# Kernel optimization log

Hardware: AMD Instinct MI355X
Metric: run time of the kernel (lower is better)

The kernel has to match this reference:

```python
import jax, jax.numpy as jnp
import numpy as np

DIM = 2048
H = 16       # num_heads
HKV = 4      # num_kv_heads
HD = DIM // H  # head_dim = 128
REP = H // HKV
ROPE_BASE = 10000.0
QK_GAIN_INIT = 1.0
B, T = 4, 2048


def rms_norm(x):
    # F.rms_norm with eps=None -> machine eps of dtype, no weight
    eps = jnp.finfo(x.dtype).eps
    return x * jax.lax.rsqrt(jnp.mean(x * x, axis=-1, keepdims=True) + eps)


def apply_rotary_emb(x, cos, sin):
    # x: [B, h, T, HD]; cos/sin: [T, HD//2]
    h = x.shape[-1] // 2
    x1, x2 = x[..., :h], x[..., h:]
    return jnp.concatenate((x1 * cos + x2 * sin, -x1 * sin + x2 * cos), axis=-1)


def setup_inputs() -> dict:
    key = jax.random.key(0)
    ks = jax.random.split(key, 6)
    kv_dim = HKV * HD
    x = jax.random.normal(ks[0], (B, T, DIM), dtype=jnp.float32)
    Wq = jax.random.normal(ks[1], (DIM, DIM), dtype=jnp.float32) * 0.02
    Wk = jax.random.normal(ks[2], (kv_dim, DIM), dtype=jnp.float32) * 0.02
    Wv = jax.random.normal(ks[3], (kv_dim, DIM), dtype=jnp.float32) * 0.02
    Wproj = jax.random.normal(ks[4], (DIM, DIM), dtype=jnp.float32) * 0.02
    q_gain = jnp.full((H,), QK_GAIN_INIT, dtype=jnp.float32)
    return {"x": x, "Wq": Wq, "Wk": Wk, "Wv": Wv, "Wproj": Wproj, "q_gain": q_gain}


def reference(x, Wq, Wk, Wv, Wproj, q_gain):
    Bs, Ts, D = x.shape
    # QKV projections (bias-free Linear: x @ W.T)
    q = (x @ Wq.T).reshape(Bs, Ts, H, HD).transpose(0, 2, 1, 3)      # [B,H,T,HD]
    k = (x @ Wk.T).reshape(Bs, Ts, HKV, HD).transpose(0, 2, 1, 3)    # [B,HKV,T,HD]
    v = (x @ Wv.T).reshape(Bs, Ts, HKV, HD).transpose(0, 2, 1, 3)
    # RMSNorm over head_dim
    q, k = rms_norm(q), rms_norm(k)
    # rotary
    inv_freq = 1.0 / (ROPE_BASE ** (jnp.arange(0, HD, 2, dtype=jnp.float32) / HD))
    t = jnp.arange(Ts, dtype=jnp.float32)
    freqs = jnp.outer(t, inv_freq)  # [T, HD//2]
    cos, sin = jnp.cos(freqs), jnp.sin(freqs)
    q = apply_rotary_emb(q, cos, sin)
    k = apply_rotary_emb(k, cos, sin)
    # per-head query gain
    q = q * q_gain[None, :, None, None]
    # GQA attention without materializing repeated K/V
    qg = q.reshape(Bs, HKV, REP, Ts, HD)
    scale = 1.0 / jnp.sqrt(jnp.asarray(HD, dtype=q.dtype))
    scores = jnp.einsum('bgrtd,bgsd->bgrts', qg, k) * scale  # [B,HKV,REP,T,T]
    causal = jnp.tril(jnp.ones((Ts, Ts), dtype=bool))
    scores = jnp.where(causal, scores, jnp.finfo(scores.dtype).min)
    attn = jax.nn.softmax(scores, axis=-1)
    y = jnp.einsum('bgrts,bgsd->bgrtd', attn, v)              # [B,HKV,REP,T,HD]
    y = y.reshape(Bs, H, Ts, HD).transpose(0, 2, 1, 3).reshape(Bs, Ts, D)
    return y @ Wproj.T
```

## Files before the change

kernel.cpp:

```cpp
#include <hip/hip_runtime.h>
#include <stdint.h>

typedef unsigned short u16;
typedef __attribute__((ext_vector_type(4))) float f32x4;
typedef __attribute__((ext_vector_type(8))) __bf16 bf16x8;
typedef __attribute__((ext_vector_type(4))) u16 u16x4;
typedef __attribute__((ext_vector_type(8))) u16 u16x8;

#define T_SEQ 2048
#define NB 4
#define NH 16
#define NKV 4
#define HDIM 128
#define PSTR 72

__device__ __forceinline__ u16 f2bf(float f) {
  __bf16 h = (__bf16)f;
  return __builtin_bit_cast(u16, h);
}
__device__ __forceinline__ float bf2f(u16 u) {
  union { uint32_t u; float f; } v; v.u = ((uint32_t)u) << 16;
  return v.f;
}
__device__ __forceinline__ void gload16(const void* g, void* l) {
  __builtin_amdgcn_global_load_lds((const __attribute__((address_space(1))) void*)g,
                                   (__attribute__((address_space(3))) void*)l, 16, 0, 0);
}
__device__ __forceinline__ f32x4 mfma16(bf16x8 a, bf16x8 b, f32x4 c) {
  return __builtin_amdgcn_mfma_f32_16x16x32_bf16(a, b, c, 0, 0, 0);
}

__global__ __launch_bounds__(256) void cvt_all(const float* __restrict__ x,
                                               const float* __restrict__ wq,
                                               const float* __restrict__ wk,
                                               const float* __restrict__ wv,
                                               const float* __restrict__ wp,
                                               u16* __restrict__ xo, u16* __restrict__ wqo,
                                               u16* __restrict__ wko, u16* __restrict__ wvo,
                                               u16* __restrict__ wpo) {
  const int C_X = 16777216 / 4, C_WQ = 4194304 / 4, C_WKV = 1048576 / 4;
  const int B1 = C_X, B2 = B1 + C_WQ, B3 = B2 + C_WKV, B4 = B3 + C_WKV;
  const int total = B4 + C_WQ;
  int idx = blockIdx.x * 256 + threadIdx.x;
  int stride = gridDim.x * 256;
  for (int c = idx; c < total; c += stride) {
    const float* src;
    u16* dst;
    int off;
    if (c < B1)      { src = x;  dst = xo;  off = c; }
    else if (c < B2) { src = wq; dst = wqo; off = c - B1; }
    else if (c < B3) { src = wk; dst = wko; off = c - B2; }
    else if (c < B4) { src = wv; dst = wvo; off = c - B3; }
    else             { src = wp; dst = wpo; off = c - B4; }
    f32x4 v = *(const f32x4*)(src + (size_t)off * 4);
    u16x4 o;
    o[0] = f2bf(v[0]); o[1] = f2bf(v[1]); o[2] = f2bf(v[2]); o[3] = f2bf(v[3]);
    *(u16x4*)(dst + (size_t)off * 4) = o;
  }
}

template <int MODE>
__global__ __launch_bounds__(256) void gemm128p3(const u16* __restrict__ A,
                                                 const u16* __restrict__ Bt,
                                                 u16* __restrict__ k_o, u16* __restrict__ v_o,
                                                 float* __restrict__ f_o,
                                                 int K, int nx, int cpx) {
  __shared__ __align__(16) u16 As3[3 * 128 * 32];
  __shared__ __align__(16) u16 Bs3[3 * 128 * 32];
  const int tid = threadIdx.x;
  const int l = tid & 63, w = tid >> 6;
  const int l15 = l & 15, g16 = l >> 4;
  const int wr = w >> 1, wc = w & 1;

  const int oid = blockIdx.x + nx * blockIdx.y;
  const int wid = (oid & 7) * cpx + (oid >> 3);
  const int m0 = (wid / nx) * 128, n0 = (wid % nx) * 128;

  f32x4 acc[4][4] = {};

  const int row0 = tid >> 2, row1 = 64 + (tid >> 2), cc = tid & 3;
  const int sc0 = cc ^ ((row0 >> 1) & 3), sc1 = cc ^ ((row1 >> 1) & 3);
  const u16* pA0 = A + (size_t)(m0 + row0) * K + sc0 * 8;
  const u16* pA1 = A + (size_t)(m0 + row1) * K + sc1 * 8;
  const u16* pB0 = Bt + (size_t)(n0 + row0) * K + sc0 * 8;
  const u16* pB1 = Bt + (size_t)(n0 + row1) * K + sc1 * 8;

#define STAGE(buf)                                                   \
  {                                                                  \
    char* ab = (char*)As3 + (buf) * 8192 + w * 1024;                 \
    char* bb = (char*)Bs3 + (buf) * 8192 + w * 1024;                 \
    gload16(pA0, ab);                                                \
    gload16(pA1, ab + 4096);                                         \
    gload16(pB0, bb);                                                \
    gload16(pB1, bb + 4096);                                         \
    pA0 += 32; pA1 += 32; pB0 += 32; pB1 += 32;                      \
  }

#define COMPUTE(buf)                                                 \
  {                                                                  \
    const u16* AsB = As3 + (buf) * 4096;                             \
    const u16* BsB = Bs3 + (buf) * 4096;                             \
    bf16x8 af[4], bfr[4];                                            \
    _Pragma("unroll")                                                \
    for (int mt = 0; mt < 4; ++mt) {                                 \
      int arow = wr * 64 + mt * 16 + l15;                            \
      af[mt] = *(const bf16x8*)&AsB[arow * 32 +                      \
                                    ((g16 ^ ((arow >> 1) & 3)) * 8)];\
    }                                                                \
    _Pragma("unroll")                                                \
    for (int nt = 0; nt < 4; ++nt) {                                 \
      int brow = wc * 64 + nt * 16 + l15;                            \
      bfr[nt] = *(const bf16x8*)&BsB[brow * 32 +                     \
                                     ((g16 ^ ((brow >> 1) & 3)) * 8)];\
    }                                                                \
    __builtin_amdgcn_s_setprio(1);                                   \
    _Pragma("unroll")                                                \
    for (int mt = 0; mt < 4; ++mt)                                   \
      _Pragma("unroll")                                              \
      for (int nt = 0; nt < 4; ++nt)                                 \
        acc[mt][nt] = mfma16(af[mt], bfr[nt], acc[mt][nt]);          \
    __builtin_amdgcn_s_setprio(0);                                   \
  }

  const int ntiles = K >> 5;
  STAGE(0);
  STAGE(1);
  asm volatile("s_waitcnt vmcnt(4)" ::: "memory");
  __builtin_amdgcn_s_barrier();

  int cur = 0, nxt = 2;
  for (int t = 0; t < ntiles; ++t) {
    const bool more2 = (t + 2 < ntiles);
    if (more2) STAGE(nxt);
    COMPUTE(cur);
    if (t + 1 < ntiles) {
      if (more2) {
        asm volatile("s_waitcnt vmcnt(4)" ::: "memory");
      } else {
        asm volatile("s_waitcnt vmcnt(0)" ::: "memory");
      }
      __builtin_amdgcn_s_barrier();
    }
    cur = (cur == 2) ? 0 : cur + 1;
    nxt = (nxt == 2) ? 0 : nxt + 1;
  }
#undef STAGE
#undef COMPUTE

#pragma unroll
  for (int mt = 0; mt < 4; ++mt) {
#pragma unroll
    for (int r = 0; r < 4; ++r) {
      int row = m0 + wr * 64 + mt * 16 + g16 * 4 + r;
#pragma unroll
      for (int nt = 0; nt < 4; ++nt) {
        int n = n0 + wc * 64 + nt * 16 + l15;
        float val = acc[mt][nt][r];
        if (MODE == 1) {
          f_o[(size_t)row * 2048 + n] = val;
        } else {
          int b = row >> 11, t = row & (T_SEQ - 1);
          u16 bv = f2bf(val);
          if (n < 512) {
            int h = n >> 7, d = n & 127;
            k_o[((size_t)(b * NKV + h) * T_SEQ + t) * HDIM + d] = bv;
          } else {
            int n2 = n - 512; int h = n2 >> 7, d = n2 & 127;
            v_o[((size_t)(b * NKV + h) * T_SEQ + t) * HDIM + d] = bv;
          }
        }
      }
    }
  }
}

template <int MODE>
__global__ __launch_bounds__(512, 2) void gemm256(const u16* __restrict__ A,
                                                  const u16* __restrict__ Bt,
                                                  u16* __restrict__ q_o,
                                                  float* __restrict__ f_o,
                                                  int K, int ntn, int cpx) {
  __shared__ __align__(16) u16 As[2][256 * 64];
  __shared__ __align__(16) u16 Bs[2][256 * 64];
  const int tid = threadIdx.x;
  const int l = tid & 63, w = tid >> 6;
  const int l16 = l & 15, g16 = l >> 4;
  const int wr = w >> 2, wc = w & 3;

  const int oid = blockIdx.x;
  const int wid = (oid & 7) * cpx + (oid >> 3);
  const int m0 = (wid / ntn) * 256, n0 = (wid % ntn) * 256;

  f32x4 acc[8][4] = {};

  const int srow = tid >> 3, scc = tid & 7;
  const u16* pA[4];
  const u16* pB[4];
#pragma unroll
  for (int j = 0; j < 4; ++j) {
    int row = j * 64 + srow;
    int cc = scc ^ (row & 7);
    pA[j] = A + (size_t)(m0 + row) * K + cc * 8;
    pB[j] = Bt + (size_t)(n0 + row) * K + cc * 8;
  }

#define STAGE(buf)                                              \
  {                                                             \
    char* ab = (char*)As[buf] + w * 1024;                       \
    char* bb = (char*)Bs[buf] + w * 1024;                       \
    _Pragma("unroll")                                           \
    for (int j = 0; j < 4; ++j) {                               \
      gload16(pA[j], ab + j * 8192);                            \
      pA[j] += 64;                                              \
    }                                                           \
    _Pragma("unroll")                                           \
    for (int j = 0; j < 4; ++j) {                               \
      gload16(pB[j], bb + j * 8192);                            \
      pB[j] += 64;                                              \
    }                                                           \
  }

  const int ntk = K >> 6;
  STAGE(0);
  __syncthreads();

  for (int t = 0; t < ntk; ++t) {
    const int buf = t & 1;
    if (t + 1 < ntk) STAGE(buf ^ 1);
#pragma unroll
    for (int ks = 0; ks < 2; ++ks) {
      bf16x8 bfr[4];
#pragma unroll
      for (int nf = 0; nf < 4; ++nf) {
        int brow = wc * 64 + nf * 16 + l16;
        int slot = (ks * 4 + g16) ^ (brow & 7);
        bfr[nf] = *(const bf16x8*)&Bs[buf][brow * 64 + slot * 8];
      }
#pragma unroll
      for (int rh = 0; rh < 2; ++rh) {
        bf16x8 af[4];
#pragma unroll
        for (int f = 0; f < 4; ++f) {
          int arow = wr * 128 + rh * 64 + f * 16 + l16;
          int slot = (ks * 4 + g16) ^ (arow & 7);
          af[f] = *(const bf16x8*)&As[buf][arow * 64 + slot * 8];
        }
        __builtin_amdgcn_s_setprio(1);
#pragma unroll
        for (int f = 0; f < 4; ++f)
#pragma unroll
          for (int nf = 0; nf < 4; ++nf)
            acc[rh * 4 + f][nf] = mfma16(af[f], bfr[nf], acc[rh * 4 + f][nf]);
        __builtin_amdgcn_s_setprio(0);
      }
    }
    __syncthreads();
  }
#undef STAGE

#pragma unroll
  for (int rf = 0; rf < 8; ++rf) {
#pragma unroll
    for (int rr = 0; rr < 4; ++rr) {
      int row = m0 + wr * 128 + rf * 16 + g16 * 4 + rr;
#pragma unroll
      for (int nf = 0; nf < 4; ++nf) {
        int n = n0 + wc * 64 + nf * 16 + l16;
        float val = acc[rf][nf][rr];
        if (MODE == 1) {
          f_o[(size_t)row * 2048 + n] = val;
        } else {
          int b = row >> 11, t = row & (T_SEQ - 1);
          int h = n >> 7, d = n & 127;
          q_o[((size_t)(b * NH + h) * T_SEQ + t) * HDIM + d] = f2bf(val);
        }
      }
    }
  }
}

__global__ __launch_bounds__(256) void rmsrope(u16* __restrict__ buf,
                                               const float* __restrict__ gains,
                                               int nheads, float fold, int useGain) {
  const int w = threadIdx.x >> 6, l = threadIdx.x & 63;
  const int rid = blockIdx.x * 4 + w;
  const int t = rid & (T_SEQ - 1);
  const int h = (rid >> 11) % nheads;
  u16* p = buf + (size_t)rid * HDIM;
  float x1 = bf2f(p[l]), x2 = bf2f(p[l + 64]);
  float ss = x1 * x1 + x2 * x2;
#pragma unroll
  for (int m = 32; m; m >>= 1) ss += __shfl_xor(ss, m, 64);
  float rn = rsqrtf(ss * (1.0f / 128.0f) + 1.1920928955078125e-7f);
  float g = useGain ? gains[h] * fold : fold;
  float sc = rn * g;
  float inv = exp2f(-(float)l * (13.287712379549449f / 64.0f));
  float ang = (float)t * inv;
  float s, c;
  __sincosf(ang, &s, &c);
  float o1 = (x1 * c + x2 * s) * sc;
  float o2 = (x2 * c - x1 * s) * sc;
  p[l] = f2bf(o1);
  p[l + 64] = f2bf(o2);
}

__global__ __launch_bounds__(256) void vtrans(const u16* __restrict__ in,
                                              u16* __restrict__ out) {
  __shared__ u16 tileT[64][PSTR];
  const int tid = threadIdx.x;
  const int t0 = blockIdx.x * 64, d0 = blockIdx.y * 64, bg = blockIdx.z;
  const int row = tid >> 2, c0 = (tid & 3) * 16;
  const u16* src = in + ((size_t)bg * T_SEQ + t0 + row) * HDIM + d0 + c0;
  u16x8 a = *(const u16x8*)src;
  u16x8 bb = *(const u16x8*)(src + 8);
#pragma unroll
  for (int j = 0; j < 8; ++j) {
    tileT[c0 + j][row] = a[j];
    tileT[c0 + 8 + j][row] = bb[j];
  }
  __syncthreads();
  u16* dst = out + ((size_t)bg * HDIM + d0 + row) * T_SEQ + t0 + c0;
  *(u16x8*)dst = *(const u16x8*)&tileT[row][c0];
  *(u16x8*)(dst + 8) = *(const u16x8*)&tileT[row][c0 + 8];
}

__global__ __launch_bounds__(512) void attn_fwd8(const u16* __restrict__ qb,
                                                 const u16* __restrict__ kb,
                                                 const u16* __restrict__ vtb,
                                                 u16* __restrict__ yb,
                                                 const float* __restrict__ gains) {
  __shared__ __align__(16) u16 Ks[64 * 128];
  __shared__ __align__(16) u16 Vs[128 * 64];
  __shared__ __align__(16) u16 Ps[8][16 * PSTR];

  const int tid = threadIdx.x, l = tid & 63, w = tid >> 6;
  const int l16 = l & 15, g16 = l >> 4;

  const int oid = blockIdx.x + 8 * blockIdx.y;
  const int wid = (oid & 7) * 64 + (oid >> 3);
  const int pair = wid & 7, bh = wid >> 3;
  const int b = bh >> 4, h = bh & 15, gr = h >> 2;

  const float Mh = 16.33f * fabsf(gains[h]) + 0.5f;
  const u16* kbase = kb + (size_t)(b * NKV + gr) * T_SEQ * HDIM;
  const u16* vtbase = vtb + (size_t)(b * NKV + gr) * HDIM * T_SEQ;

  bf16x8 ones;
#pragma unroll
  for (int j = 0; j < 8; ++j) ones[j] = (__bf16)1.0f;

  const int krow0 = tid >> 4, kc0 = tid & 15;
  const int krow1 = 32 + (tid >> 4);
  const u16* kp0_base = kbase + (size_t)krow0 * HDIM + (kc0 ^ (krow0 & 7)) * 8;
  const u16* kp1_base = kbase + (size_t)krow1 * HDIM + (kc0 ^ (krow1 & 7)) * 8;
  const int vrow0 = tid >> 3, vc0 = tid & 7;
  const int vrow1 = 64 + (tid >> 3);
  const u16* vp0_base = vtbase + (size_t)vrow0 * T_SEQ + (vc0 ^ (vrow0 & 7)) * 8;
  const u16* vp1_base = vtbase + (size_t)vrow1 * T_SEQ + (vc0 ^ (vrow1 & 7)) * 8;
  char* kd0 = (char*)Ks + (w * 64) * 16;
  char* kd1 = (char*)Ks + (512 + w * 64) * 16;
  char* vd0 = (char*)Vs + (w * 64) * 16;
  char* vd1 = (char*)Vs + (512 + w * 64) * 16;

  for (int phase = 0; phase < 2; ++phase) {
    const int qt = phase ? (15 - pair) : pair;
    const int q0 = qt * 128 + w * 16;
    const int qhi = q0 + 15;

    bf16x8 qf[4];
    const u16* qbase = qb + ((size_t)bh * T_SEQ + q0) * HDIM;
#pragma unroll
    for (int s = 0; s < 4; ++s)
      qf[s] = *(const bf16x8*)(qbase + (size_t)l16 * HDIM + s * 32 + g16 * 8);

    f32x4 oacc[8] = {};
    f32x4 dden = {};
    const int ntile = 2 * qt + 2;

    const u16* kp0 = kp0_base;
    const u16* kp1 = kp1_base;
    const u16* vp0 = vp0_base;
    const u16* vp1 = vp1_base;

    for (int kt = 0; kt < ntile; ++kt) {
      gload16(kp0, kd0);
      gload16(kp1, kd1);
      gload16(vp0, vd0);
      gload16(vp1, vd1);
      kp0 += 64 * HDIM; kp1 += 64 * HDIM;
      vp0 += 64; vp1 += 64;
      __syncthreads();

      if (kt * 64 <= qhi) {
        f32x4 sacc[4] = {};
        __builtin_amdgcn_s_setprio(1);
#pragma unroll
        for (int mt = 0; mt < 4; ++mt) {
          int key = mt * 16 + l16;
#pragma unroll
          for (int s = 0; s < 4; ++s) {
            bf16x8 kf = *(const bf16x8*)&Ks[key * 128 + ((s * 4 + g16) ^ (key & 7)) * 8];
            sacc[mt] = mfma16(kf, qf[s], sacc[mt]);
          }
        }
        __builtin_amdgcn_s_setprio(0);

        if (kt * 64 + 63 > q0) {
#pragma unroll
          for (int mt = 0; mt < 4; ++mt) {
            int keyb = kt * 64 + mt * 16 + g16 * 4;
            u16x4 p4;
#pragma unroll
            for (int r = 0; r < 4; ++r) {
              float pv = exp2f(sacc[mt][r] - Mh);
              if (keyb + r > q0 + l16) pv = 0.f;
              p4[r] = f2bf(pv);
            }
            *(u16x4*)&Ps[w][l16 * PSTR + mt * 16 + g16 * 4] = p4;
          }
        } else {
#pragma unroll
          for (int mt = 0; mt < 4; ++mt) {
            u16x4 p4;
#pragma unroll
            for (int r = 0; r < 4; ++r)
              p4[r] = f2bf(exp2f(sacc[mt][r] - Mh));
            *(u16x4*)&Ps[w][l16 * PSTR + mt * 16 + g16 * 4] = p4;
          }
        }

        __builtin_amdgcn_s_setprio(1);
#pragma unroll
        for (int ks = 0; ks < 2; ++ks) {
          bf16x8 pa = *(const bf16x8*)&Ps[w][l16 * PSTR + ks * 32 + g16 * 8];
          dden = mfma16(pa, ones, dden);
#pragma unroll
          for (int dt = 0; dt < 8; ++dt) {
            int d = dt * 16 + l16;
            bf16x8 vv = *(const bf16x8*)&Vs[d * 64 + (((ks * 4 + g16) ^ (d & 7)) * 8)];
            oacc[dt] = mfma16(pa, vv, oacc[dt]);
          }
        }
        __builtin_amdgcn_s_setprio(0);
      }
      __syncthreads();
    }

    float rden[4];
#pragma unroll
    for (int r = 0; r < 4; ++r) rden[r] = 1.f / dden[r];

#pragma unroll
    for (int dt = 0; dt < 8; ++dt)
#pragma unroll
      for (int r = 0; r < 4; ++r) {
        int t = q0 + g16 * 4 + r;
        int d = dt * 16 + l16;
        yb[(((size_t)b * T_SEQ + t) * NH + h) * HDIM + d] = f2bf(oacc[dt][r] * rden[r]);
      }
    __syncthreads();
  }
}

extern "C" void kernel_launch(void* const* d_in, const int* in_sizes, int n_in,
                              void* d_out, int out_size, void* d_ws, size_t ws_size,
                              hipStream_t stream) {
  const float* x = (const float*)d_in[0];
  const float* Wq = (const float*)d_in[1];
  const float* Wk = (const float*)d_in[2];
  const float* Wv = (const float*)d_in[3];
  const float* Wproj = (const float*)d_in[4];
  const float* qg = (const float*)d_in[5];
  float* out = (float*)d_out;

  u16* xbf = (u16*)d_ws;
  u16* Wqkv = xbf + (size_t)8192 * 2048;
  u16* Wpj = Wqkv + (size_t)3072 * 2048;
  u16* qbuf = Wpj + (size_t)2048 * 2048;
  u16* kbuf = qbuf + (size_t)8192 * 2048;
  u16* vbuf = kbuf + (size_t)2048 * 2048;
  u16* ybuf = xbf;
  u16* vtbuf = Wqkv;

  cvt_all<<<2048, 256, 0, stream>>>(x, Wq, Wk, Wv, Wproj,
                                    xbf, Wqkv, Wqkv + (size_t)2048 * 2048,
                                    Wqkv + (size_t)2560 * 2048, Wpj);

  gemm256<0><<<256, 512, 0, stream>>>(xbf, Wqkv, qbuf, nullptr, 2048, 8, 32);

  gemm128p3<2><<<dim3(8, 64), 256, 0, stream>>>(xbf, Wqkv + (size_t)2048 * 2048,
                                                kbuf, vbuf, nullptr, 2048, 8, 64);

  rmsrope<<<32768, 256, 0, stream>>>(qbuf, qg, NH,
                                     1.4426950408889634f / 11.313708498984761f, 1);
  rmsrope<<<8192, 256, 0, stream>>>(kbuf, nullptr, NKV, 1.0f, 0);
  vtrans<<<dim3(32, 2, 16), 256, 0, stream>>>(vbuf, vtbuf);

  attn_fwd8<<<dim3(8, 64), 512, 0, stream>>>(qbuf, kbuf, vtbuf, ybuf, qg);

  gemm256<1><<<256, 512, 0, stream>>>(ybuf, Wpj, nullptr, out, 2048, 8, 32);
}
```

Baseline: 346.0 us.

## Double-buffer K tiles in attention and merge rmsrope/vtrans launches

The attention kernel now double-buffers K in shared memory, issuing the next K tile's global-to-LDS load before computing on the current one, with explicit vmcnt waits and raw barriers in place of __syncthreads. V stays single-buffered and is reloaded after each tile. The aim is to hide K load latency behind MFMA work. Separately, the two rmsrope launches and the vtrans launch are folded into one postproc kernel to save launch overhead. The costs are extra LDS per block and a hand-written wait/barrier schedule that depends on exact counts of outstanding loads.

```diff
diff --git a/kernel.cpp b/kernel.cpp
--- a/kernel.cpp
+++ b/kernel.cpp
@@ -279,57 +279,63 @@
   }
 }
 
-__global__ __launch_bounds__(256) void rmsrope(u16* __restrict__ buf,
-                                               const float* __restrict__ gains,
-                                               int nheads, float fold, int useGain) {
-  const int w = threadIdx.x >> 6, l = threadIdx.x & 63;
-  const int rid = blockIdx.x * 4 + w;
-  const int t = rid & (T_SEQ - 1);
-  const int h = (rid >> 11) % nheads;
-  u16* p = buf + (size_t)rid * HDIM;
-  float x1 = bf2f(p[l]), x2 = bf2f(p[l + 64]);
-  float ss = x1 * x1 + x2 * x2;
-#pragma unroll
-  for (int m = 32; m; m >>= 1) ss += __shfl_xor(ss, m, 64);
-  float rn = rsqrtf(ss * (1.0f / 128.0f) + 1.1920928955078125e-7f);
-  float g = useGain ? gains[h] * fold : fold;
-  float sc = rn * g;
-  float inv = exp2f(-(float)l * (13.287712379549449f / 64.0f));
-  float ang = (float)t * inv;
-  float s, c;
-  __sincosf(ang, &s, &c);
-  float o1 = (x1 * c + x2 * s) * sc;
-  float o2 = (x2 * c - x1 * s) * sc;
-  p[l] = f2bf(o1);
-  p[l + 64] = f2bf(o2);
-}
-
-__global__ __launch_bounds__(256) void vtrans(const u16* __restrict__ in,
-                                              u16* __restrict__ out) {
-  __shared__ u16 tileT[64][PSTR];
-  const int tid = threadIdx.x;
-  const int t0 = blockIdx.x * 64, d0 = blockIdx.y * 64, bg = blockIdx.z;
-  const int row = tid >> 2, c0 = (tid & 3) * 16;
-  const u16* src = in + ((size_t)bg * T_SEQ + t0 + row) * HDIM + d0 + c0;
-  u16x8 a = *(const u16x8*)src;
-  u16x8 bb = *(const u16x8*)(src + 8);
-#pragma unroll
-  for (int j = 0; j < 8; ++j) {
-    tileT[c0 + j][row] = a[j];
-    tileT[c0 + 8 + j][row] = bb[j];
-  }
-  __syncthreads();
-  u16* dst = out + ((size_t)bg * HDIM + d0 + row) * T_SEQ + t0 + c0;
-  *(u16x8*)dst = *(const u16x8*)&tileT[row][c0];
-  *(u16x8*)(dst + 8) = *(const u16x8*)&tileT[row][c0 + 8];
-}
-
-__global__ __launch_bounds__(512) void attn_fwd8(const u16* __restrict__ qb,
+__global__ __launch_bounds__(256) void postproc(u16* __restrict__ qbuf,
+                                                u16* __restrict__ kbuf,
+                                                const u16* __restrict__ vbuf,
+                                                u16* __restrict__ vtbuf,
+                                                const float* __restrict__ gains) {
+  const int bid = blockIdx.x;
+  if (bid < 40960) {
+    const bool isq = (bid < 32768);
+    u16* buf = isq ? qbuf : kbuf;
+    const int base = isq ? bid : (bid - 32768);
+    const int w = threadIdx.x >> 6, l = threadIdx.x & 63;
+    const int rid = base * 4 + w;
+    const int t = rid & (T_SEQ - 1);
+    const int h = (rid >> 11) % (isq ? NH : NKV);
+    u16* p = buf + (size_t)rid * HDIM;
+    float x1 = bf2f(p[l]), x2 = bf2f(p[l + 64]);
+    float ss = x1 * x1 + x2 * x2;
+#pragma unroll
+    for (int m = 32; m; m >>= 1) ss += __shfl_xor(ss, m, 64);
+    float rn = rsqrtf(ss * (1.0f / 128.0f) + 1.1920928955078125e-7f);
+    float g = isq ? gains[h] * (1.4426950408889634f / 11.313708498984761f) : 1.0f;
+    float sc = rn * g;
+    float inv = exp2f(-(float)l * (13.287712379549449f / 64.0f));
+    float ang = (float)t * inv;
+    float s, c;
+    __sincosf(ang, &s, &c);
+    float o1 = (x1 * c + x2 * s) * sc;
+    float o2 = (x2 * c - x1 * s) * sc;
+    p[l] = f2bf(o1);
+    p[l + 64] = f2bf(o2);
+  } else {
+    __shared__ u16 tileT[64][PSTR];
+    const int tidx = bid - 40960;
+    const int t0 = (tidx & 31) * 64, d0 = ((tidx >> 5) & 1) * 64, bg = tidx >> 6;
+    const int tid = threadIdx.x;
+    const int row = tid >> 2, c0 = (tid & 3) * 16;
+    const u16* src = vbuf + ((size_t)bg * T_SEQ + t0 + row) * HDIM + d0 + c0;
+    u16x8 a = *(const u16x8*)src;
+    u16x8 bb = *(const u16x8*)(src + 8);
+#pragma unroll
+    for (int j = 0; j < 8; ++j) {
+      tileT[c0 + j][row] = a[j];
+      tileT[c0 + 8 + j][row] = bb[j];
+    }
+    __syncthreads();
+    u16* dst = vtbuf + ((size_t)bg * HDIM + d0 + row) * T_SEQ + t0 + c0;
+    *(u16x8*)dst = *(const u16x8*)&tileT[row][c0];
+    *(u16x8*)(dst + 8) = *(const u16x8*)&tileT[row][c0 + 8];
+  }
+}
+
+__global__ __launch_bounds__(512) void attn_fwd9(const u16* __restrict__ qb,
                                                  const u16* __restrict__ kb,
                                                  const u16* __restrict__ vtb,
                                                  u16* __restrict__ yb,
                                                  const float* __restrict__ gains) {
-  __shared__ __align__(16) u16 Ks[64 * 128];
+  __shared__ __align__(16) u16 Ks[2][64 * 128];
   __shared__ __align__(16) u16 Vs[128 * 64];
   __shared__ __align__(16) u16 Ps[8][16 * PSTR];
 
@@ -357,10 +363,77 @@
   const int vrow1 = 64 + (tid >> 3);
   const u16* vp0_base = vtbase + (size_t)vrow0 * T_SEQ + (vc0 ^ (vrow0 & 7)) * 8;
   const u16* vp1_base = vtbase + (size_t)vrow1 * T_SEQ + (vc0 ^ (vrow1 & 7)) * 8;
-  char* kd0 = (char*)Ks + (w * 64) * 16;
-  char* kd1 = (char*)Ks + (512 + w * 64) * 16;
   char* vd0 = (char*)Vs + (w * 64) * 16;
   char* vd1 = (char*)Vs + (512 + w * 64) * 16;
+
+#define STAGEK(bf)                                                   \
+  {                                                                  \
+    gload16(kp0, (char*)&Ks[bf][0] + (w * 64) * 16);                 \
+    gload16(kp1, (char*)&Ks[bf][0] + ((512 + w * 64)) * 16);         \
+    kp0 += 64 * HDIM;                                                \
+    kp1 += 64 * HDIM;                                                \
+  }
+#define STAGEV()                                                     \
+  {                                                                  \
+    gload16(vp0, vd0);                                               \
+    gload16(vp1, vd1);                                               \
+    vp0 += 64;                                                       \
+    vp1 += 64;                                                       \
+  }
+
+#define ATT_TILE(KT, KSBUF)                                                \
+  if ((KT) * 64 <= qhi) {                                                  \
+    f32x4 sacc[4] = {};                                                    \
+    __builtin_amdgcn_s_setprio(1);                                         \
+    _Pragma("unroll")                                                      \
+    for (int mt = 0; mt < 4; ++mt) {                                       \
+      int key = mt * 16 + l16;                                             \
+      _Pragma("unroll")                                                    \
+      for (int s = 0; s < 4; ++s) {                                        \
+        bf16x8 kf = *(const bf16x8*)&Ks[KSBUF][key * 128 +                 \
+                                    (((s * 4 + g16) ^ (key & 7)) * 8)];    \
+        sacc[mt] = mfma16(kf, qf[s], sacc[mt]);                            \
+      }                                                                    \
+    }                                                                      \
+    __builtin_amdgcn_s_setprio(0);                                         \
+    if ((KT) * 64 + 63 > q0) {                                             \
+      _Pragma("unroll")                                                    \
+      for (int mt = 0; mt < 4; ++mt) {                                     \
+        int keyb = (KT) * 64 + mt * 16 + g16 * 4;                          \
+        u16x4 p4;                                                          \
+        _Pragma("unroll")                                                  \
+        for (int r = 0; r < 4; ++r) {                                      \
+          float pv = exp2f(sacc[mt][r] - Mh);                              \
+          if (keyb + r > q0 + l16) pv = 0.f;                               \
+          p4[r] = f2bf(pv);                                                \
+        }                                                                  \
+        *(u16x4*)&Ps[w][l16 * PSTR + mt * 16 + g16 * 4] = p4;              \
+      }                                                                    \
+    } else {                                                               \
+      _Pragma("unroll")                                                    \
+      for (int mt = 0; mt < 4; ++mt) {                                     \
+        u16x4 p4;                                                          \
+        _Pragma("unroll")                                                  \
+        for (int r = 0; r < 4; ++r)                                        \
+          p4[r] = f2bf(exp2f(sacc[mt][r] - Mh));                           \
+        *(u16x4*)&Ps[w][l16 * PSTR + mt * 16 + g16 * 4] = p4;              \
+      }                                                                    \
+    }                                                                      \
+    __builtin_amdgcn_s_setprio(1);                                         \
+    _Pragma("unroll")                                                      \
+    for (int ks = 0; ks < 2; ++ks) {                                       \
+      bf16x8 pa = *(const bf16x8*)&Ps[w][l16 * PSTR + ks * 32 + g16 * 8];  \
+      dden = mfma16(pa, ones, dden);                                       \
+      _Pragma("unroll")                                                    \
+      for (int dt = 0; dt < 8; ++dt) {                                     \
+        int d = dt * 16 + l16;                                             \
+        bf16x8 vv = *(const bf16x8*)&Vs[d * 64 +                           \
+                                    (((ks * 4 + g16) ^ (d & 7)) * 8)];     \
+        oacc[dt] = mfma16(pa, vv, oacc[dt]);                               \
+      }                                                                    \
+    }                                                                      \
+    __builtin_amdgcn_s_setprio(0);                                         \
+  }
 
   for (int phase = 0; phase < 2; ++phase) {
     const int qt = phase ? (15 - pair) : pair;
@@ -382,68 +455,28 @@
     const u16* vp0 = vp0_base;
     const u16* vp1 = vp1_base;
 
-    for (int kt = 0; kt < ntile; ++kt) {
-      gload16(kp0, kd0);
-      gload16(kp1, kd1);
-      gload16(vp0, vd0);
-      gload16(vp1, vd1);
-      kp0 += 64 * HDIM; kp1 += 64 * HDIM;
-      vp0 += 64; vp1 += 64;
-      __syncthreads();
-
-      if (kt * 64 <= qhi) {
-        f32x4 sacc[4] = {};
-        __builtin_amdgcn_s_setprio(1);
-#pragma unroll
-        for (int mt = 0; mt < 4; ++mt) {
-          int key = mt * 16 + l16;
-#pragma unroll
-          for (int s = 0; s < 4; ++s) {
-            bf16x8 kf = *(const bf16x8*)&Ks[key * 128 + ((s * 4 + g16) ^ (key & 7)) * 8];
-            sacc[mt] = mfma16(kf, qf[s], sacc[mt]);
-          }
-        }
-        __builtin_amdgcn_s_setprio(0);
-
-        if (kt * 64 + 63 > q0) {
-#pragma unroll
-          for (int mt = 0; mt < 4; ++mt) {
-            int keyb = kt * 64 + mt * 16 + g16 * 4;
-            u16x4 p4;
-#pragma unroll
-            for (int r = 0; r < 4; ++r) {
-              float pv = exp2f(sacc[mt][r] - Mh);
-              if (keyb + r > q0 + l16) pv = 0.f;
-              p4[r] = f2bf(pv);
-            }
-            *(u16x4*)&Ps[w][l16 * PSTR + mt * 16 + g16 * 4] = p4;
-          }
-        } else {
-#pragma unroll
-          for (int mt = 0; mt < 4; ++mt) {
-            u16x4 p4;
-#pragma unroll
-            for (int r = 0; r < 4; ++r)
-              p4[r] = f2bf(exp2f(sacc[mt][r] - Mh));
-            *(u16x4*)&Ps[w][l16 * PSTR + mt * 16 + g16 * 4] = p4;
-          }
-        }
-
-        __builtin_amdgcn_s_setprio(1);
-#pragma unroll
-        for (int ks = 0; ks < 2; ++ks) {
-          bf16x8 pa = *(const bf16x8*)&Ps[w][l16 * PSTR + ks * 32 + g16 * 8];
-          dden = mfma16(pa, ones, dden);
-#pragma unroll
-          for (int dt = 0; dt < 8; ++dt) {
-            int d = dt * 16 + l16;
-            bf16x8 vv = *(const bf16x8*)&Vs[d * 64 + (((ks * 4 + g16) ^ (d & 7)) * 8)];
-            oacc[dt] = mfma16(pa, vv, oacc[dt]);
-          }
-        }
-        __builtin_amdgcn_s_setprio(0);
-      }
-      __syncthreads();
+    STAGEK(0);
+    STAGEV();
+
+    for (int kt = 0; kt < ntile; kt += 2) {
+      STAGEK(1);
+      asm volatile("s_waitcnt vmcnt(2)" ::: "memory");
+      __builtin_amdgcn_s_barrier();
+      ATT_TILE(kt, 0);
+      __builtin_amdgcn_s_barrier();
+      STAGEV();
+
+      const bool more = (kt + 2 < ntile);
+      if (more) STAGEK(0);
+      if (more) {
+        asm volatile("s_waitcnt vmcnt(2)" ::: "memory");
+      } else {
+        asm volatile("s_waitcnt vmcnt(0)" ::: "memory");
+      }
+      __builtin_amdgcn_s_barrier();
+      ATT_TILE(kt + 1, 1);
+      __builtin_amdgcn_s_barrier();
+      if (more) STAGEV();
     }
 
     float rden[4];
@@ -460,6 +493,9 @@
       }
     __syncthreads();
   }
+#undef STAGEK
+#undef STAGEV
+#undef ATT_TILE
 }
 
 extern "C" void kernel_launch(void* const* d_in, const int* in_sizes, int n_in,
@@ -491,12 +527,9 @@
   gemm128p3<2><<<dim3(8, 64), 256, 0, stream>>>(xbf, Wqkv + (size_t)2048 * 2048,
                                                 kbuf, vbuf, nullptr, 2048, 8, 64);
 
-  rmsrope<<<32768, 256, 0, stream>>>(qbuf, qg, NH,
-                                     1.4426950408889634f / 11.313708498984761f, 1);
-  rmsrope<<<8192, 256, 0, stream>>>(kbuf, nullptr, NKV, 1.0f, 0);
-  vtrans<<<dim3(32, 2, 16), 256, 0, stream>>>(vbuf, vtbuf);
-
-  attn_fwd8<<<dim3(8, 64), 512, 0, stream>>>(qbuf, kbuf, vtbuf, ybuf, qg);
+  postproc<<<41984, 256, 0, stream>>>(qbuf, kbuf, vbuf, vtbuf, qg);
+
+  attn_fwd9<<<dim3(8, 64), 512, 0, stream>>>(qbuf, kbuf, vtbuf, ybuf, qg);
 
   gemm256<1><<<256, 512, 0, stream>>>(ybuf, Wpj, nullptr, out, 2048, 8, 32);
 }
```

Result: slower. 361.5 us (+4.5%).
